# Kernel optimization log

Hardware: AMD Instinct MI355X
Metric: run time of the kernel (lower is better)

Reference implementation:

```python
import jax, jax.numpy as jnp
import numpy as np

HID = 2048
NK, DK = 16, 128        # key heads, key head dim
NV, DV = 32, 128        # value heads, value head dim
KC = 4                  # conv kernel
P = NV // NK            # value heads per key head
SV = P * DV             # state value dim (256)
QD = NK * DK
VD = NV * DV
QKV = QD + QD + VD      # 8192
B, T = 2, 2048
EPS_NORM = 1e-12        # F.normalize eps
EPS_RMS = 1e-6


def _l2norm(x):
    n = jnp.sqrt(jnp.sum(x * x, axis=-1, keepdims=True))
    return x / jnp.maximum(n, EPS_NORM)


def setup_inputs() -> dict:
    key = jax.random.key(0)
    ks = jax.random.split(key, 8)
    lin = lambda k, o, i: jax.random.normal(k, (o, i), jnp.float32) / np.sqrt(i).astype(np.float32)
    return {
        "x": jax.random.normal(ks[0], (B, T, HID), jnp.float32),
        "W_qkv": lin(ks[1], QKV, HID),
        "W_z": lin(ks[2], VD, HID),
        "W_b": lin(ks[3], NV, HID),
        "W_a": lin(ks[4], NV, HID),
        "conv_w": jax.random.normal(ks[5], (QKV, KC), jnp.float32) * 0.1,  # depthwise kernel
        "dt_bias": jnp.zeros((NV,), jnp.float32),
        "A_log": jnp.zeros((NV,), jnp.float32),
        "norm_w": jnp.ones((DV,), jnp.float32),
        "W_out": lin(ks[6], HID, VD),
    }


def reference(x, W_qkv, W_z, W_b, W_a, conv_w, dt_bias, A_log, norm_w, W_out):
    Bq, Tq, _ = x.shape
    qkv = jnp.einsum('btc,dc->btd', x, W_qkv)        # [B,T,QKV]
    z = jnp.einsum('btc,dc->btd', x, W_z)            # [B,T,VD]
    beta = jax.nn.sigmoid(jnp.einsum('btc,hc->bth', x, W_b))           # [B,T,NV]
    dt = jax.nn.softplus(jnp.einsum('btc,hc->bth', x, W_a) + dt_bias)  # [B,T,NV]
    decay = jnp.exp(-dt * jnp.exp(A_log))                               # [B,T,NV]

    # causal depthwise conv1d (groups = channels), zero left-pad of KC-1
    xp = jnp.pad(qkv, ((0, 0), (KC - 1, 0), (0, 0)))                    # [B,T+KC-1,QKV]
    qkv_c = sum(xp[:, j:j + Tq, :] * conv_w[:, j] for j in range(KC))   # [B,T,QKV]
    new_conv_buf = jnp.transpose(xp[:, -(KC - 1):, :], (0, 2, 1))        # [B,QKV,KC-1]

    q = _l2norm(qkv_c[..., :QD].reshape(Bq, Tq, NK, DK))
    k = _l2norm(qkv_c[..., QD:2 * QD].reshape(Bq, Tq, NK, DK))
    v = qkv_c[..., 2 * QD:].reshape(Bq, Tq, NK, P, DV)
    beta_r = beta.reshape(Bq, Tq, NK, P)
    decay_r = decay.reshape(Bq, Tq, NK, P)

    # time-major for scan
    qT = jnp.swapaxes(q, 0, 1)
    kT = jnp.swapaxes(k, 0, 1)
    vT = jnp.swapaxes(v, 0, 1)
    bT = jnp.swapaxes(beta_r, 0, 1)
    dT = jnp.swapaxes(decay_r, 0, 1)

    def step(S, inp):  # S: [B,NK,DK,P,DV]
        q_t, k_t, v_t, b_t, d_t = inp
        Sk = jnp.einsum('bhi,bhipj->bhpj', k_t, S)          # read old state
        dv = b_t[..., None] * (v_t - Sk)                     # beta-weighted delta
        upd = jnp.einsum('bhi,bhpj->bhipj', k_t, dv)
        S = S * d_t[:, :, None, :, None] + upd               # gated decay + rank-1 update
        o = jnp.einsum('bhi,bhipj->bhpj', q_t, S)
        return S, o

    S0 = jnp.zeros((Bq, NK, DK, P, DV), x.dtype)
    S_final, outs = jax.lax.scan(step, S0, (qT, kT, vT, bT, dT))
    out = jnp.swapaxes(outs, 0, 1).reshape(Bq, Tq, NV, DV)   # [B,T,NV,DV]

    # RMSNorm over value head dim
    rms = jax.lax.rsqrt(jnp.mean(out * out, axis=-1, keepdims=True) + EPS_RMS)
    out = out * rms * norm_w
    out = out.reshape(Bq, Tq, VD) * jax.nn.silu(z)
    y = jnp.einsum('btd,cd->btc', out, W_out)                # [B,T,HID]
    return y, S_final.reshape(Bq, NK, DK, SV), new_conv_buf
```

## Files before the change

kernel.cpp:

```cpp
#include <hip/hip_runtime.h>

#define B_ 2
#define T_ 2048
#define HID_ 2048
#define NK_ 16
#define DK_ 128
#define NV_ 32
#define DV_ 128
#define QKV_ 8192
#define VD_ 4096
#define QD_ 2048
#define MM (B_*T_)
#define SV_ 256

typedef unsigned short u16;
typedef __attribute__((ext_vector_type(8))) unsigned short u16x8;
typedef __attribute__((ext_vector_type(8))) __bf16 bf16x8;
typedef __attribute__((ext_vector_type(4))) float f32x4;

__device__ inline u16 f2bf(float f) {
    unsigned int x = __float_as_uint(f);
    x += 0x7fffu + ((x >> 16) & 1u);
    return (u16)(x >> 16);
}
__device__ inline float bf2f(u16 v) {
    return __uint_as_float(((unsigned int)v) << 16);
}

__global__ __launch_bounds__(256) void k_cast(const float* __restrict__ in,
                                              u16* __restrict__ out, int n4) {
    int i = blockIdx.x * 256 + threadIdx.x;
    if (i >= n4) return;
    float4 v = ((const float4*)in)[i];
    ((ushort4*)out)[i] = make_ushort4(f2bf(v.x), f2bf(v.y), f2bf(v.z), f2bf(v.w));
}

template <int OUT_BF16>
__global__ __launch_bounds__(256) void k_gemm_bt(const u16* __restrict__ A,
                                                 const u16* __restrict__ Bm,
                                                 void* __restrict__ Cv,
                                                 int M, int N, int K) {
    __shared__ __align__(16) u16 As[128 * 72];
    __shared__ __align__(16) u16 Bs[128 * 72];
    int nbx = N >> 7;
    int bx = blockIdx.x % nbx, by = blockIdx.x / nbx;
    int brow = by << 7, bcol = bx << 7;
    int tid = threadIdx.x, lane = tid & 63, w = tid >> 6;
    int wr = (w >> 1) << 6, wc = (w & 1) << 6;
    int srow = tid >> 1, scol = (tid & 1) << 5;

    const u16* ag = A + (size_t)(brow + srow) * K + scol;
    const u16* bg = Bm + (size_t)(bcol + srow) * K + scol;
    u16* asw = &As[srow * 72 + scol];
    u16* bsw = &Bs[srow * 72 + scol];

    f32x4 acc[4][4];
#pragma unroll
    for (int m = 0; m < 4; m++)
#pragma unroll
        for (int n = 0; n < 4; n++) acc[m][n] = (f32x4){0.f, 0.f, 0.f, 0.f};

    int lrow = lane & 15, khalf = (lane >> 4) * 8;

    for (int kt = 0; kt < K; kt += 64) {
#pragma unroll
        for (int u = 0; u < 4; ++u) {
            *(u16x8*)(asw + u * 8) = *(const u16x8*)(ag + kt + u * 8);
            *(u16x8*)(bsw + u * 8) = *(const u16x8*)(bg + kt + u * 8);
        }
        __syncthreads();
#pragma unroll
        for (int kk = 0; kk < 64; kk += 32) {
            bf16x8 af[4], bfr[4];
#pragma unroll
            for (int m = 0; m < 4; m++)
                af[m] = *(const bf16x8*)&As[(wr + m * 16 + lrow) * 72 + kk + khalf];
#pragma unroll
            for (int n = 0; n < 4; n++)
                bfr[n] = *(const bf16x8*)&Bs[(wc + n * 16 + lrow) * 72 + kk + khalf];
#pragma unroll
            for (int m = 0; m < 4; m++)
#pragma unroll
                for (int n = 0; n < 4; n++)
                    acc[m][n] = __builtin_amdgcn_mfma_f32_16x16x32_bf16(af[m], bfr[n], acc[m][n], 0, 0, 0);
        }
        __syncthreads();
    }
    int crow = brow + wr + (lane >> 4) * 4;
    int ccol = bcol + wc + lrow;
#pragma unroll
    for (int m = 0; m < 4; m++)
#pragma unroll
        for (int n = 0; n < 4; n++) {
            if (OUT_BF16) {
                u16* cp = (u16*)Cv + (size_t)(crow + m * 16) * N + ccol + n * 16;
#pragma unroll
                for (int r = 0; r < 4; r++) cp[(size_t)r * N] = f2bf(acc[m][n][r]);
            } else {
                float* cp = (float*)Cv + (size_t)(crow + m * 16) * N + ccol + n * 16;
#pragma unroll
                for (int r = 0; r < 4; r++) cp[(size_t)r * N] = acc[m][n][r];
            }
        }
}

__global__ __launch_bounds__(256) void k_bd(const float* __restrict__ x,
                                            const float* __restrict__ Wb,
                                            const float* __restrict__ Wa,
                                            const float* __restrict__ dtb,
                                            const float* __restrict__ Alog,
                                            float* __restrict__ beta,
                                            float* __restrict__ decay) {
    int h2 = threadIdx.x & 63;
    int bt = blockIdx.x * 4 + (threadIdx.x >> 6);
    const float* xr = x + (size_t)bt * HID_;
    const float* W = (h2 < NV_) ? (Wb + (size_t)h2 * HID_) : (Wa + (size_t)(h2 - NV_) * HID_);
    float acc = 0.f;
    for (int kk = 0; kk < HID_; kk += 4) {
        float4 xv = *(const float4*)&xr[kk];
        float4 wv = *(const float4*)&W[kk];
        acc += xv.x * wv.x + xv.y * wv.y + xv.z * wv.z + xv.w * wv.w;
    }
    if (h2 < NV_) {
        beta[(size_t)bt * NV_ + h2] = 1.f / (1.f + expf(-acc));
    } else {
        int hh = h2 - NV_;
        float a = acc + dtb[hh];
        float sp = (a > 20.f) ? a : log1pf(expf(a));
        decay[(size_t)bt * NV_ + hh] = expf(-sp * expf(Alog[hh]));
    }
}

__global__ __launch_bounds__(128) void k_conv_norm(const u16* __restrict__ qkv,
                                                   const float* __restrict__ conv_w,
                                                   u16* __restrict__ qn,
                                                   u16* __restrict__ kn,
                                                   u16* __restrict__ vv) {
    int g = blockIdx.x & 63;
    int bt = blockIdx.x >> 6;
    int t = bt & (T_ - 1);
    int ch = (g << 7) + threadIdx.x;
    float4 wv = *(const float4*)&conv_w[(size_t)ch << 2];
    const u16* col = qkv + (size_t)(bt - t) * QKV_ + ch;
    float s = bf2f(col[(size_t)t * QKV_]) * wv.w;
    if (t >= 1) s += bf2f(col[(size_t)(t - 1) * QKV_]) * wv.z;
    if (t >= 2) s += bf2f(col[(size_t)(t - 2) * QKV_]) * wv.y;
    if (t >= 3) s += bf2f(col[(size_t)(t - 3) * QKV_]) * wv.x;

    if (g < 32) {
        float ss = s * s;
#pragma unroll
        for (int m = 1; m < 64; m <<= 1) ss += __shfl_xor(ss, m);
        __shared__ float red[2];
        if ((threadIdx.x & 63) == 0) red[threadIdx.x >> 6] = ss;
        __syncthreads();
        float tot = red[0] + red[1];
        float sc = 1.f / fmaxf(sqrtf(tot), 1e-12f);
        float o = s * sc;
        if (g < 16) qn[((size_t)bt * NK_ + g) * DK_ + threadIdx.x] = f2bf(o);
        else        kn[((size_t)bt * NK_ + (g - 16)) * DK_ + threadIdx.x] = f2bf(o);
    } else {
        vv[((size_t)bt * NV_ + (g - 32)) * DV_ + threadIdx.x] = f2bf(s);
    }
}

__global__ __launch_bounds__(256) void k_convbuf(const u16* __restrict__ qkv,
                                                 float* __restrict__ ob) {
    int idx = blockIdx.x * 256 + threadIdx.x;
    if (idx >= B_ * QKV_ * 3) return;
    int jj = idx % 3;
    int d = (idx / 3) & (QKV_ - 1);
    int b = idx / (3 * QKV_);
    ob[idx] = bf2f(qkv[((size_t)b * T_ + (T_ - 3 + jj)) * QKV_ + d]);
}

__global__ __launch_bounds__(256) void k_scan(const u16* __restrict__ qn,
                                              const u16* __restrict__ kn,
                                              const u16* __restrict__ vv,
                                              const float* __restrict__ beta,
                                              const float* __restrict__ decay,
                                              float* __restrict__ attn,
                                              float* __restrict__ Sout) {
    int cg = blockIdx.x & 7;
    int h = (blockIdx.x >> 3) & 15;
    int b = blockIdx.x >> 7;
    int tid = threadIdx.x;
    int cl = tid >> 3;
    int oi = tid & 7;
    int i0 = oi << 4;
    int c = (cg << 5) + cl;
    int p = c >> 7;
    int j = c & 127;
    int nv = (h << 1) + p;

    __shared__ __align__(16) float sk[2][160];
    __shared__ __align__(16) float sq[2][160];
    __shared__ __align__(16) float sv[2][32];

    float S[16];
#pragma unroll
    for (int ii = 0; ii < 16; ++ii) S[ii] = 0.f;

    const size_t bT = (size_t)b * T_;
    if (tid < 128) sk[0][(tid >> 4) * 20 + (tid & 15)] = bf2f(kn[((bT) * NK_ + h) * DK_ + tid]);
    else { int q_ = tid - 128; sq[0][(q_ >> 4) * 20 + (q_ & 15)] = bf2f(qn[((bT) * NK_ + h) * DK_ + q_]); }
    if (tid < 32) sv[0][tid] = bf2f(vv[((bT) * NV_ + nv) * DV_ + ((cg & 3) << 5) + tid]);
    __syncthreads();

    int buf = 0;
    for (int t = 0; t < T_; ++t) {
        float kreg[16], qreg[16];
        const float4* k4 = (const float4*)&sk[buf][oi * 20];
        const float4* q4 = (const float4*)&sq[buf][oi * 20];
#pragma unroll
        for (int u = 0; u < 4; ++u) {
            float4 kv = k4[u], qv = q4[u];
            kreg[u * 4 + 0] = kv.x; kreg[u * 4 + 1] = kv.y; kreg[u * 4 + 2] = kv.z; kreg[u * 4 + 3] = kv.w;
            qreg[u * 4 + 0] = qv.x; qreg[u * 4 + 1] = qv.y; qreg[u * 4 + 2] = qv.z; qreg[u * 4 + 3] = qv.w;
        }
        float vval = sv[buf][cl];
        float bt_s = beta[(bT + t) * NV_ + nv];
        float dc_s = decay[(bT + t) * NV_ + nv];

        float skp = 0.f;
#pragma unroll
        for (int ii = 0; ii < 16; ++ii) skp += kreg[ii] * S[ii];
        skp += __shfl_xor(skp, 1);
        skp += __shfl_xor(skp, 2);
        skp += __shfl_xor(skp, 4);

        float dv = bt_s * (vval - skp);
        float op = 0.f;
#pragma unroll
        for (int ii = 0; ii < 16; ++ii) {
            float sn = S[ii] * dc_s + kreg[ii] * dv;
            S[ii] = sn;
            op += qreg[ii] * sn;
        }
        op += __shfl_xor(op, 1);
        op += __shfl_xor(op, 2);
        op += __shfl_xor(op, 4);

        int tn = t + 1;
        if (tn < T_) {
            int nb = buf ^ 1;
            if (tid < 128) sk[nb][(tid >> 4) * 20 + (tid & 15)] = bf2f(kn[((bT + tn) * NK_ + h) * DK_ + tid]);
            else { int q_ = tid - 128; sq[nb][(q_ >> 4) * 20 + (q_ & 15)] = bf2f(qn[((bT + tn) * NK_ + h) * DK_ + q_]); }
            if (tid < 32) sv[nb][tid] = bf2f(vv[((bT + tn) * NV_ + nv) * DV_ + ((cg & 3) << 5) + tid]);
        }
        if (oi == 0) attn[((bT + t) * NV_ + nv) * DV_ + j] = op;
        __syncthreads();
        buf ^= 1;
    }
#pragma unroll
    for (int ii = 0; ii < 16; ++ii)
        Sout[(((size_t)b * NK_ + h) * DK_ + (i0 + ii)) * SV_ + c] = S[ii];
}

__global__ __launch_bounds__(256) void k_rms_silu(const float* __restrict__ attn,
                                                  const u16* __restrict__ z,
                                                  const float* __restrict__ norm_w,
                                                  u16* __restrict__ ofuse) {
    int w = threadIdx.x >> 6, lane = threadIdx.x & 63;
    size_t hm = (size_t)blockIdx.x * 4 + w;
    const float* row = attn + hm * DV_;
    float2 v = *(const float2*)&row[lane * 2];
    float ss = v.x * v.x + v.y * v.y;
#pragma unroll
    for (int m = 1; m < 64; m <<= 1) ss += __shfl_xor(ss, m);
    float rms = rsqrtf(ss * (1.f / DV_) + 1e-6f);
    float2 nw = *(const float2*)&norm_w[lane * 2];
    size_t idx = hm * DV_ + lane * 2;
    ushort2 zv2 = *(const ushort2*)&z[idx];
    float z0 = bf2f(zv2.x), z1 = bf2f(zv2.y);
    float s0 = z0 / (1.f + expf(-z0));
    float s1 = z1 / (1.f + expf(-z1));
    *(ushort2*)&ofuse[idx] = make_ushort2(f2bf(v.x * rms * nw.x * s0),
                                          f2bf(v.y * rms * nw.y * s1));
}

extern "C" void kernel_launch(void* const* d_in, const int* in_sizes, int n_in,
                              void* d_out, int out_size, void* d_ws, size_t ws_size,
                              hipStream_t stream) {
    const float* x     = (const float*)d_in[0];
    const float* Wqkv  = (const float*)d_in[1];
    const float* Wz    = (const float*)d_in[2];
    const float* Wb    = (const float*)d_in[3];
    const float* Wa    = (const float*)d_in[4];
    const float* convw = (const float*)d_in[5];
    const float* dtb   = (const float*)d_in[6];
    const float* Alog  = (const float*)d_in[7];
    const float* normw = (const float*)d_in[8];
    const float* Wout  = (const float*)d_in[9];
    float* out = (float*)d_out;

    char* ws = (char*)d_ws;
    u16*   x_bf    = (u16*)(ws + ((size_t)0 << 20));
    u16*   Wqkv_bf = (u16*)(ws + ((size_t)16 << 20));
    u16*   vv      = (u16*)(ws + ((size_t)16 << 20));
    u16*   Wout_bf = (u16*)(ws + ((size_t)16 << 20));
    u16*   Wz_bf   = (u16*)(ws + ((size_t)48 << 20));
    float* beta    = (float*)(ws + ((size_t)48 << 20));
    float* decay   = (float*)(ws + ((size_t)48 << 20) + (1 << 19));
    u16*   qkv_bf  = (u16*)(ws + ((size_t)64 << 20));
    float* attn    = (float*)(ws + ((size_t)64 << 20));
    u16*   z_bf    = (u16*)(ws + ((size_t)128 << 20));
    u16*   qn      = (u16*)(ws + ((size_t)160 << 20));
    u16*   kn      = (u16*)(ws + ((size_t)176 << 20));
    u16*   ofuse   = (u16*)(ws + ((size_t)160 << 20));

    float* y_out = out;
    float* S_out = out + (size_t)MM * HID_;
    float* cbuf  = S_out + (size_t)B_ * NK_ * DK_ * SV_;

    k_cast<<<dim3((MM * HID_ / 4 + 255) / 256), 256, 0, stream>>>(x, x_bf, MM * HID_ / 4);
    k_cast<<<dim3((QKV_ * HID_ / 4 + 255) / 256), 256, 0, stream>>>(Wqkv, Wqkv_bf, QKV_ * HID_ / 4);
    k_cast<<<dim3((VD_ * HID_ / 4 + 255) / 256), 256, 0, stream>>>(Wz, Wz_bf, VD_ * HID_ / 4);

    k_gemm_bt<1><<<dim3((MM / 128) * (QKV_ / 128)), 256, 0, stream>>>(x_bf, Wqkv_bf, qkv_bf, MM, QKV_, HID_);
    k_gemm_bt<1><<<dim3((MM / 128) * (VD_ / 128)), 256, 0, stream>>>(x_bf, Wz_bf, z_bf, MM, VD_, HID_);

    k_bd<<<dim3(MM / 4), 256, 0, stream>>>(x, Wb, Wa, dtb, Alog, beta, decay);

    k_conv_norm<<<dim3(MM * 64), 128, 0, stream>>>(qkv_bf, convw, qn, kn, vv);
    k_convbuf<<<dim3((B_ * QKV_ * 3 + 255) / 256), 256, 0, stream>>>(qkv_bf, cbuf);

    k_scan<<<dim3(256), 256, 0, stream>>>(qn, kn, vv, beta, decay, attn, S_out);

    k_cast<<<dim3((HID_ * VD_ / 4 + 255) / 256), 256, 0, stream>>>(Wout, Wout_bf, HID_ * VD_ / 4);

    k_rms_silu<<<dim3(MM * NV_ / 4), 256, 0, stream>>>(attn, z_bf, normw, ofuse);

    k_gemm_bt<0><<<dim3((MM / 128) * (HID_ / 128)), 256, 0, stream>>>(ofuse, Wout_bf, y_out, MM, HID_, VD_);
}
```

Before: 2.823 ms.

## Restructure delta-rule scan with register prefetch and precomputed q·k output

The scan drops its shared-memory double buffer and per-step __syncthreads. Each thread now prefetches its own q/k slices, v, beta, decay and q·k values two steps ahead in registers. The output is computed algebraically as decay*(q·S) + (q·k)*dv, so both dot products run in one pass over the old state. This relies on a new k_qk kernel that precomputes q·k per head and timestep. Normalized q/k are stored in fp32 rather than bf16, which doubles their memory traffic but removes the per-step conversions. The Wout cast and workspace layout are also reshuffled, which must not alias live buffers.

```diff
diff --git a/kernel.cpp b/kernel.cpp
--- a/kernel.cpp
+++ b/kernel.cpp
@@ -133,8 +133,8 @@
 
 __global__ __launch_bounds__(128) void k_conv_norm(const u16* __restrict__ qkv,
                                                    const float* __restrict__ conv_w,
-                                                   u16* __restrict__ qn,
-                                                   u16* __restrict__ kn,
+                                                   float* __restrict__ qn,
+                                                   float* __restrict__ kn,
                                                    u16* __restrict__ vv) {
     int g = blockIdx.x & 63;
     int bt = blockIdx.x >> 6;
@@ -157,8 +157,8 @@
         float tot = red[0] + red[1];
         float sc = 1.f / fmaxf(sqrtf(tot), 1e-12f);
         float o = s * sc;
-        if (g < 16) qn[((size_t)bt * NK_ + g) * DK_ + threadIdx.x] = f2bf(o);
-        else        kn[((size_t)bt * NK_ + (g - 16)) * DK_ + threadIdx.x] = f2bf(o);
+        if (g < 16) qn[((size_t)bt * NK_ + g) * DK_ + threadIdx.x] = o;
+        else        kn[((size_t)bt * NK_ + (g - 16)) * DK_ + threadIdx.x] = o;
     } else {
         vv[((size_t)bt * NV_ + (g - 32)) * DV_ + threadIdx.x] = f2bf(s);
     }
@@ -174,13 +174,67 @@
     ob[idx] = bf2f(qkv[((size_t)b * T_ + (T_ - 3 + jj)) * QKV_ + d]);
 }
 
-__global__ __launch_bounds__(256) void k_scan(const u16* __restrict__ qn,
-                                              const u16* __restrict__ kn,
-                                              const u16* __restrict__ vv,
-                                              const float* __restrict__ beta,
-                                              const float* __restrict__ decay,
-                                              float* __restrict__ attn,
-                                              float* __restrict__ Sout) {
+__global__ __launch_bounds__(256) void k_qk(const float* __restrict__ qn,
+                                            const float* __restrict__ kn,
+                                            float* __restrict__ qk) {
+    int w = threadIdx.x >> 6, lane = threadIdx.x & 63;
+    int bh = blockIdx.x * 4 + w;
+    float2 q2 = *(const float2*)&qn[(size_t)bh * DK_ + lane * 2];
+    float2 k2 = *(const float2*)&kn[(size_t)bh * DK_ + lane * 2];
+    float s = q2.x * k2.x + q2.y * k2.y;
+#pragma unroll
+    for (int m = 1; m < 64; m <<= 1) s += __shfl_xor(s, m);
+    if (lane == 0) qk[bh] = s;
+}
+
+#define SCAN_BODY(s, tcur)                                                    \
+  {                                                                           \
+    float kv[16], qv[16];                                                     \
+    _Pragma("unroll") for (int u = 0; u < 4; ++u) {                           \
+      *(f32x4*)&kv[u * 4] = skv##s[u];                                        \
+      *(f32x4*)&qv[u * 4] = sqv##s[u];                                        \
+    }                                                                         \
+    float vval = bf2f(svv##s);                                                \
+    float be = sbe##s, dc = sdc##s, qks = sqk##s;                             \
+    if ((tcur) + 2 < T_) {                                                    \
+      _Pragma("unroll") for (int u = 0; u < 4; ++u) {                         \
+        skv##s[u] = *(const f32x4*)(kpre + u * 4);                            \
+        sqv##s[u] = *(const f32x4*)(qpre + u * 4);                            \
+      }                                                                       \
+      svv##s = *vpre; sbe##s = *bpre; sdc##s = *dpre; sqk##s = *qkpre;        \
+      kpre += NK_ * DK_; qpre += NK_ * DK_; vpre += NV_ * DV_;                \
+      bpre += NV_; dpre += NV_; qkpre += NK_;                                 \
+    }                                                                         \
+    float gS[16];                                                             \
+    _Pragma("unroll") for (int ii = 0; ii < 16; ++ii) gS[ii] = dc * S[ii];    \
+    float a0 = 0, a1 = 0, a2 = 0, a3 = 0, b0 = 0, b1 = 0, b2 = 0, b3 = 0;    \
+    _Pragma("unroll") for (int u = 0; u < 4; ++u) {                           \
+      a0 = fmaf(kv[u*4+0], S[u*4+0], a0); b0 = fmaf(qv[u*4+0], S[u*4+0], b0); \
+      a1 = fmaf(kv[u*4+1], S[u*4+1], a1); b1 = fmaf(qv[u*4+1], S[u*4+1], b1); \
+      a2 = fmaf(kv[u*4+2], S[u*4+2], a2); b2 = fmaf(qv[u*4+2], S[u*4+2], b2); \
+      a3 = fmaf(kv[u*4+3], S[u*4+3], a3); b3 = fmaf(qv[u*4+3], S[u*4+3], b3); \
+    }                                                                         \
+    float skp = (a0 + a1) + (a2 + a3);                                        \
+    float qs = (b0 + b1) + (b2 + b3);                                         \
+    skp += __shfl_xor(skp, 1); qs += __shfl_xor(qs, 1);                       \
+    skp += __shfl_xor(skp, 2); qs += __shfl_xor(qs, 2);                       \
+    skp += __shfl_xor(skp, 4); qs += __shfl_xor(qs, 4);                       \
+    float dv = be * (vval - skp);                                             \
+    float o = fmaf(qks, dv, dc * qs);                                         \
+    _Pragma("unroll") for (int ii = 0; ii < 16; ++ii)                         \
+      S[ii] = fmaf(kv[ii], dv, gS[ii]);                                       \
+    if (oi == 0) *ao = o;                                                     \
+    ao += NV_ * DV_;                                                          \
+  }
+
+__global__ __launch_bounds__(256, 1) void k_scan(const float* __restrict__ qn,
+                                                 const float* __restrict__ kn,
+                                                 const u16* __restrict__ vv,
+                                                 const float* __restrict__ beta,
+                                                 const float* __restrict__ decay,
+                                                 const float* __restrict__ qk,
+                                                 float* __restrict__ attn,
+                                                 float* __restrict__ Sout) {
     int cg = blockIdx.x & 7;
     int h = (blockIdx.x >> 3) & 15;
     int b = blockIdx.x >> 7;
@@ -192,66 +246,47 @@
     int p = c >> 7;
     int j = c & 127;
     int nv = (h << 1) + p;
-
-    __shared__ __align__(16) float sk[2][160];
-    __shared__ __align__(16) float sq[2][160];
-    __shared__ __align__(16) float sv[2][32];
+    const size_t bT = (size_t)b * T_;
 
     float S[16];
 #pragma unroll
     for (int ii = 0; ii < 16; ++ii) S[ii] = 0.f;
 
-    const size_t bT = (size_t)b * T_;
-    if (tid < 128) sk[0][(tid >> 4) * 20 + (tid & 15)] = bf2f(kn[((bT) * NK_ + h) * DK_ + tid]);
-    else { int q_ = tid - 128; sq[0][(q_ >> 4) * 20 + (q_ & 15)] = bf2f(qn[((bT) * NK_ + h) * DK_ + q_]); }
-    if (tid < 32) sv[0][tid] = bf2f(vv[((bT) * NV_ + nv) * DV_ + ((cg & 3) << 5) + tid]);
-    __syncthreads();
-
-    int buf = 0;
-    for (int t = 0; t < T_; ++t) {
-        float kreg[16], qreg[16];
-        const float4* k4 = (const float4*)&sk[buf][oi * 20];
-        const float4* q4 = (const float4*)&sq[buf][oi * 20];
-#pragma unroll
-        for (int u = 0; u < 4; ++u) {
-            float4 kv = k4[u], qv = q4[u];
-            kreg[u * 4 + 0] = kv.x; kreg[u * 4 + 1] = kv.y; kreg[u * 4 + 2] = kv.z; kreg[u * 4 + 3] = kv.w;
-            qreg[u * 4 + 0] = qv.x; qreg[u * 4 + 1] = qv.y; qreg[u * 4 + 2] = qv.z; qreg[u * 4 + 3] = qv.w;
-        }
-        float vval = sv[buf][cl];
-        float bt_s = beta[(bT + t) * NV_ + nv];
-        float dc_s = decay[(bT + t) * NV_ + nv];
-
-        float skp = 0.f;
-#pragma unroll
-        for (int ii = 0; ii < 16; ++ii) skp += kreg[ii] * S[ii];
-        skp += __shfl_xor(skp, 1);
-        skp += __shfl_xor(skp, 2);
-        skp += __shfl_xor(skp, 4);
-
-        float dv = bt_s * (vval - skp);
-        float op = 0.f;
-#pragma unroll
-        for (int ii = 0; ii < 16; ++ii) {
-            float sn = S[ii] * dc_s + kreg[ii] * dv;
-            S[ii] = sn;
-            op += qreg[ii] * sn;
-        }
-        op += __shfl_xor(op, 1);
-        op += __shfl_xor(op, 2);
-        op += __shfl_xor(op, 4);
-
-        int tn = t + 1;
-        if (tn < T_) {
-            int nb = buf ^ 1;
-            if (tid < 128) sk[nb][(tid >> 4) * 20 + (tid & 15)] = bf2f(kn[((bT + tn) * NK_ + h) * DK_ + tid]);
-            else { int q_ = tid - 128; sq[nb][(q_ >> 4) * 20 + (q_ & 15)] = bf2f(qn[((bT + tn) * NK_ + h) * DK_ + q_]); }
-            if (tid < 32) sv[nb][tid] = bf2f(vv[((bT + tn) * NV_ + nv) * DV_ + ((cg & 3) << 5) + tid]);
-        }
-        if (oi == 0) attn[((bT + t) * NV_ + nv) * DV_ + j] = op;
-        __syncthreads();
-        buf ^= 1;
-    }
+    const float* kbase = kn + ((bT)*NK_ + h) * DK_ + i0;
+    const float* qbase = qn + ((bT)*NK_ + h) * DK_ + i0;
+    const u16*   vbase = vv + ((bT)*NV_ + nv) * DV_ + j;
+    const float* bbase = beta + (bT)*NV_ + nv;
+    const float* dbase = decay + (bT)*NV_ + nv;
+    const float* qkbase = qk + (bT)*NK_ + h;
+    float* ao = attn + ((bT)*NV_ + nv) * DV_ + j;
+
+    f32x4 skv0[4], sqv0[4], skv1[4], sqv1[4];
+    u16 svv0, svv1;
+    float sbe0, sdc0, sqk0, sbe1, sdc1, sqk1;
+#pragma unroll
+    for (int u = 0; u < 4; ++u) {
+        skv0[u] = *(const f32x4*)(kbase + u * 4);
+        sqv0[u] = *(const f32x4*)(qbase + u * 4);
+        skv1[u] = *(const f32x4*)(kbase + NK_ * DK_ + u * 4);
+        sqv1[u] = *(const f32x4*)(qbase + NK_ * DK_ + u * 4);
+    }
+    svv0 = vbase[0]; svv1 = vbase[NV_ * DV_];
+    sbe0 = bbase[0]; sbe1 = bbase[NV_];
+    sdc0 = dbase[0]; sdc1 = dbase[NV_];
+    sqk0 = qkbase[0]; sqk1 = qkbase[NK_];
+
+    const float* kpre = kbase + 2 * NK_ * DK_;
+    const float* qpre = qbase + 2 * NK_ * DK_;
+    const u16*   vpre = vbase + 2 * NV_ * DV_;
+    const float* bpre = bbase + 2 * NV_;
+    const float* dpre = dbase + 2 * NV_;
+    const float* qkpre = qkbase + 2 * NK_;
+
+    for (int t = 0; t < T_; t += 2) {
+        SCAN_BODY(0, t)
+        SCAN_BODY(1, t + 1)
+    }
+
 #pragma unroll
     for (int ii = 0; ii < 16; ++ii)
         Sout[(((size_t)b * NK_ + h) * DK_ + (i0 + ii)) * SV_ + c] = S[ii];
@@ -295,19 +330,20 @@
     float* out = (float*)d_out;
 
     char* ws = (char*)d_ws;
-    u16*   x_bf    = (u16*)(ws + ((size_t)0 << 20));
+    u16*   x_bf    = (u16*)(ws);
+    float* beta    = (float*)(ws);
+    float* decay   = (float*)(ws + ((size_t)1 << 19));
+    float* qk      = (float*)(ws + ((size_t)1 << 20));
     u16*   Wqkv_bf = (u16*)(ws + ((size_t)16 << 20));
     u16*   vv      = (u16*)(ws + ((size_t)16 << 20));
-    u16*   Wout_bf = (u16*)(ws + ((size_t)16 << 20));
     u16*   Wz_bf   = (u16*)(ws + ((size_t)48 << 20));
-    float* beta    = (float*)(ws + ((size_t)48 << 20));
-    float* decay   = (float*)(ws + ((size_t)48 << 20) + (1 << 19));
+    u16*   Wout_bf = (u16*)(ws + ((size_t)48 << 20));
     u16*   qkv_bf  = (u16*)(ws + ((size_t)64 << 20));
     float* attn    = (float*)(ws + ((size_t)64 << 20));
     u16*   z_bf    = (u16*)(ws + ((size_t)128 << 20));
-    u16*   qn      = (u16*)(ws + ((size_t)160 << 20));
-    u16*   kn      = (u16*)(ws + ((size_t)176 << 20));
+    float* qn      = (float*)(ws + ((size_t)160 << 20));
     u16*   ofuse   = (u16*)(ws + ((size_t)160 << 20));
+    float* kn      = (float*)(ws + ((size_t)192 << 20));
 
     float* y_out = out;
     float* S_out = out + (size_t)MM * HID_;
@@ -320,14 +356,15 @@
     k_gemm_bt<1><<<dim3((MM / 128) * (QKV_ / 128)), 256, 0, stream>>>(x_bf, Wqkv_bf, qkv_bf, MM, QKV_, HID_);
     k_gemm_bt<1><<<dim3((MM / 128) * (VD_ / 128)), 256, 0, stream>>>(x_bf, Wz_bf, z_bf, MM, VD_, HID_);
 
+    k_cast<<<dim3((HID_ * VD_ / 4 + 255) / 256), 256, 0, stream>>>(Wout, Wout_bf, HID_ * VD_ / 4);
     k_bd<<<dim3(MM / 4), 256, 0, stream>>>(x, Wb, Wa, dtb, Alog, beta, decay);
 
     k_conv_norm<<<dim3(MM * 64), 128, 0, stream>>>(qkv_bf, convw, qn, kn, vv);
     k_convbuf<<<dim3((B_ * QKV_ * 3 + 255) / 256), 256, 0, stream>>>(qkv_bf, cbuf);
 
-    k_scan<<<dim3(256), 256, 0, stream>>>(qn, kn, vv, beta, decay, attn, S_out);
-
-    k_cast<<<dim3((HID_ * VD_ / 4 + 255) / 256), 256, 0, stream>>>(Wout, Wout_bf, HID_ * VD_ / 4);
+    k_qk<<<dim3(MM * NK_ / 4), 256, 0, stream>>>(qn, kn, qk);
+
+    k_scan<<<dim3(256), 256, 0, stream>>>(qn, kn, vv, beta, decay, qk, attn, S_out);
 
     k_rms_silu<<<dim3(MM * NV_ / 4), 256, 0, stream>>>(attn, z_bf, normw, ofuse);
 
```

Result: faster. 2.274 ms (-19.5%).
